# Kernel tuning notes

Measured on AMD Instinct MI355X. Metric: run time of the kernel, lower is better.

The kernel has to match this reference:

```python
import jax, jax.numpy as jnp
import numpy as np

B, T, DI, D = 8, 256, 64, 128
PRED_LEN, OUT_DIM = 96, 7
LN_EPS = 1e-5


def setup_inputs() -> dict:
    key = jax.random.key(0)
    ks = jax.random.split(key, 10)
    s = lambda k, shape, sc: (jax.random.normal(k, shape, jnp.float32) * sc)
    return {
        'x': s(ks[0], (B, T, DI), 1.0),
        'W_b': s(ks[1], (DI, D), DI ** -0.5), 'b_b': jnp.zeros((D,), jnp.float32),
        'Wk': s(ks[2], (D, D), D ** -0.5),
        'Wv': s(ks[3], (D, D), D ** -0.5),
        'Wq': s(ks[4], (D, D), D ** -0.5),
        'W_m': s(ks[5], (D, 3), D ** -0.5), 'b_m': jnp.zeros((3,), jnp.float32),
        'W_f': s(ks[6], (2 * D, D), (2 * D) ** -0.5), 'b_f': jnp.zeros((D,), jnp.float32),
        'W1': s(ks[7], (D, D), D ** -0.5), 'b1': jnp.zeros((D,), jnp.float32),
        'g1': jnp.ones((D,), jnp.float32), 'be1': jnp.zeros((D,), jnp.float32),
        'W2': s(ks[8], (D, PRED_LEN * OUT_DIM), D ** -0.5),
        'b2': jnp.zeros((PRED_LEN * OUT_DIM,), jnp.float32),
    }


def _layernorm(h, g, b):
    mu = h.mean(-1, keepdims=True)
    var = jnp.mean((h - mu) ** 2, -1, keepdims=True)
    return (h - mu) * jax.lax.rsqrt(var + LN_EPS) * g + b


def _forward(x, W_b, b_b, Wk, Wv, Wq, W_m, b_m, W_f, b_f, W1, b1, g1, be1, W2, b2):
    # Backbone P: feature extraction -> f_t  [B,T,D]
    f = jax.nn.gelu(x @ W_b + b_b)
    # Meta-learner: per-step (theta_t, eta_t, alpha_t)
    meta = jax.nn.sigmoid(f @ W_m + b_m)               # [B,T,3]
    theta = 0.01 * meta[..., 0]                         # learning rate
    eta = meta[..., 1]                                  # momentum
    alpha = 0.1 * meta[..., 2]                          # forget/decay
    # Key/value/query projections (precomputed; recurrence is in M,S only)
    k = f @ Wk; v = f @ Wv; q = f @ Wq                  # [B,T,D] each
    seq = (jnp.swapaxes(k, 0, 1), jnp.swapaxes(v, 0, 1), jnp.swapaxes(q, 0, 1),
           theta.T, eta.T, alpha.T)                     # time-major
    M0 = jnp.zeros((B, D, D), f.dtype)
    S0 = jnp.zeros((B, D, D), f.dtype)

    def step(carry, inp):
        M, S = carry
        kt, vt, qt, th, et, al = inp
        # grad of 0.5*||M k - v||^2 wrt M  (rank-1 outer product)
        err = jnp.einsum('bij,bj->bi', M, kt) - vt
        grad = jnp.einsum('bi,bj->bij', err, kt)
        S = et[:, None, None] * S - th[:, None, None] * grad
        M = (1.0 - al)[:, None, None] * M + S
        m_t = jnp.einsum('bij,bj->bi', M, qt)           # retrieve
        return (M, S), m_t

    (_, _), m_seq = jax.lax.scan(step, (M0, S0), seq)
    m = jnp.swapaxes(m_seq, 0, 1)                       # [B,T,D]
    # Gated fusion
    gate = jax.nn.sigmoid(jnp.concatenate([f, m], -1) @ W_f + b_f)
    fused = f * gate + m * (1.0 - gate)
    # Prediction head on last timestep (dropout=0 / eval)
    last = fused[:, -1, :]
    h = jax.nn.gelu(_layernorm(last @ W1 + b1, g1, be1))
    out = h @ W2 + b2
    return out.reshape(B, PRED_LEN, OUT_DIM)


def reference(x, W_b, b_b, Wk, Wv, Wq, W_m, b_m, W_f, b_f, W1, b1, g1, be1, W2, b2):
    return _forward(x, W_b, b_b, Wk, Wv, Wq, W_m, b_m, W_f, b_f, W1, b1, g1, be1, W2, b2)
```

## Files before the change

kernel.cpp:

```cpp
#include <hip/hip_runtime.h>
#include <hip/hip_bf16.h>

#define BB 8
#define TT 256
#define DIN 64
#define DD 128

__device__ __forceinline__ float gelu_tanh(float x) {
  float x3 = x * x * x;
  return 0.5f * x * (1.0f + tanhf(0.7978845608028654f * (x + 0.044715f * x3)));
}
__device__ __forceinline__ float sigmoidf(float x) {
  return 1.0f / (1.0f + __expf(-x));
}

template <typename T> __device__ __forceinline__ float getv(const void* p, int i);
template <> __device__ __forceinline__ float getv<float>(const void* p, int i) {
  return ((const float*)p)[i];
}
template <> __device__ __forceinline__ float getv<__hip_bfloat16>(const void* p, int i) {
  return __bfloat162float(((const __hip_bfloat16*)p)[i]);
}

template <typename T>
__device__ __forceinline__ void fmaV(float* acc, uint4 wv, float fc);
template <>
__device__ __forceinline__ void fmaV<float>(float* acc, uint4 wv, float fc) {
  acc[0] += fc * __uint_as_float(wv.x);
  acc[1] += fc * __uint_as_float(wv.y);
  acc[2] += fc * __uint_as_float(wv.z);
  acc[3] += fc * __uint_as_float(wv.w);
}
template <>
__device__ __forceinline__ void fmaV<__hip_bfloat16>(float* acc, uint4 wv,
                                                     float fc) {
  const unsigned int u0 = wv.x, u1 = wv.y, u2 = wv.z, u3 = wv.w;
  acc[0] += fc * __uint_as_float(u0 << 16);
  acc[1] += fc * __uint_as_float(u0 & 0xffff0000u);
  acc[2] += fc * __uint_as_float(u1 << 16);
  acc[3] += fc * __uint_as_float(u1 & 0xffff0000u);
  acc[4] += fc * __uint_as_float(u2 << 16);
  acc[5] += fc * __uint_as_float(u2 & 0xffff0000u);
  acc[6] += fc * __uint_as_float(u3 << 16);
  acc[7] += fc * __uint_as_float(u3 & 0xffff0000u);
}

template <int CTRL>
__device__ __forceinline__ float dpp_add(float x) {
  int s = __builtin_amdgcn_update_dpp(0, __float_as_int(x), CTRL, 0xF, 0xF, true);
  return x + __int_as_float(s);
}

__device__ __forceinline__ float rowsum16(float p) {
  p = dpp_add<0xB1>(p);
  p = dpp_add<0x4E>(p);
  p = dpp_add<0x124>(p);
  p = dpp_add<0x128>(p);
  return p;
}

__device__ __forceinline__ void gload_lds16(const void* g, void* l) {
  __builtin_amdgcn_global_load_lds(
      (const __attribute__((address_space(1))) void*)g,
      (__attribute__((address_space(3))) void*)l, 16, 0, 0);
}

__device__ __forceinline__ int dtype_good(const unsigned short* u, int idx) {
  unsigned int bits = ((unsigned int)u[idx]) << 16;
  float f = __uint_as_float(bits);
  float a = fabsf(f);
  return (a == 0.0f || (a > 1e-4f && a < 100.0f)) ? 1 : 0;
}

template <typename T>
__device__ void k1_body(const void* x, const void* W_b, const void* b_b,
                        const void* Wk, const void* Wv, const void* Wq,
                        const void* W_m, const void* b_m,
                        float* kout, float* vout, float* scal4,
                        float* q_last, float* f_last) {
  constexpr int VEC = (sizeof(T) == 2) ? 8 : 4;
  constexpr int OC = DD / VEC;
  constexpr int SPL = 128 / OC;
  const int row = blockIdx.x;
  const int b = row >> 8, t = row & 255;
  const int tid = threadIdx.x;
  const int oc = tid % OC, s = tid / OC;

  __shared__ float xs[DIN];
  __shared__ float fs[DD];
  __shared__ float partA[128 * DD / 16];
  __shared__ float partB[128 * DD / 16];

  if (tid < DIN) xs[tid] = getv<T>(x, row * DIN + tid);
  __syncthreads();

  float acc[VEC];

#define GEMV_PART(Wp, SRC, R, PART)                                          \
  {                                                                          \
    _Pragma("unroll") for (int j = 0; j < VEC; ++j) acc[j] = 0.0f;           \
    constexpr int rps = (R) / SPL;                                           \
    _Pragma("unroll 4") for (int cc = 0; cc < rps; ++cc) {                   \
      const int c = s * rps + cc;                                            \
      const uint4 wv =                                                       \
          *(const uint4*)((const T*)(Wp) + (size_t)c * DD + oc * VEC);       \
      fmaV<T>(acc, wv, (SRC)[c]);                                            \
    }                                                                        \
    _Pragma("unroll") for (int j = 0; j < VEC; ++j)                          \
        (PART)[s * DD + oc * VEC + j] = acc[j];                              \
  }

  GEMV_PART(W_b, xs, DIN, partA);
  __syncthreads();
  if (tid < DD) {
    float a = getv<T>(b_b, tid);
#pragma unroll
    for (int ss = 0; ss < SPL; ++ss) a += partA[ss * DD + tid];
    fs[tid] = gelu_tanh(a);
  }
  __syncthreads();

  GEMV_PART(Wk, fs, DD, partA);
  GEMV_PART(Wv, fs, DD, partB);
  __syncthreads();
  if (tid < DD) {
    float ak = 0.0f, av = 0.0f;
#pragma unroll
    for (int ss = 0; ss < SPL; ++ss) {
      ak += partA[ss * DD + tid];
      av += partB[ss * DD + tid];
    }
    kout[row * DD + tid] = ak;
    vout[row * DD + tid] = av;
  }

  if (tid < 64) {
    float a3[3];
#pragma unroll
    for (int j = 0; j < 3; ++j) {
      float pj = fs[tid] * getv<T>(W_m, tid * 3 + j) +
                 fs[tid + 64] * getv<T>(W_m, (tid + 64) * 3 + j);
      pj = rowsum16(pj);
      pj += __shfl_xor(pj, 16);
      pj += __shfl_xor(pj, 32);
      a3[j] = pj;
    }
    if (tid == 0) {
      scal4[row * 4 + 0] = 0.01f * sigmoidf(a3[0] + getv<T>(b_m, 0));
      scal4[row * 4 + 1] = sigmoidf(a3[1] + getv<T>(b_m, 1));
      scal4[row * 4 + 2] = 0.1f * sigmoidf(a3[2] + getv<T>(b_m, 2));
      scal4[row * 4 + 3] = 0.0f;
    }
  }

  if (t == TT - 1) {
    __syncthreads();
    GEMV_PART(Wq, fs, DD, partA);
    __syncthreads();
    if (tid < DD) {
      float aq = 0.0f;
#pragma unroll
      for (int ss = 0; ss < SPL; ++ss) aq += partA[ss * DD + tid];
      q_last[b * DD + tid] = aq;
      f_last[b * DD + tid] = fs[tid];
    }
  }
#undef GEMV_PART
}

__global__ __launch_bounds__(128) void k1_kern(
    const void* x, const void* W_b, const void* b_b, const void* Wk,
    const void* Wv, const void* Wq, const void* W_m, const void* b_m,
    float* kout, float* vout, float* scal4, float* q_last, float* f_last) {
  __shared__ int gcnt[2];
  {
    const int tid = threadIdx.x;
    const unsigned short* u = (const unsigned short*)x;
    int good = 0;
#pragma unroll
    for (int j = 0; j < 16; ++j) good += dtype_good(u, j * 128 + tid);
    float gf = (float)good;
    gf = rowsum16(gf);
    gf += __shfl_xor(gf, 16);
    gf += __shfl_xor(gf, 32);
    if ((tid & 63) == 0) gcnt[tid >> 6] = (int)(gf + 0.5f);
  }
  __syncthreads();
  const bool isbf16 = (gcnt[0] + gcnt[1] >= 1536);
  __syncthreads();

  if (isbf16)
    k1_body<__hip_bfloat16>(x, W_b, b_b, Wk, Wv, Wq, W_m, b_m, kout, vout,
                            scal4, q_last, f_last);
  else
    k1_body<float>(x, W_b, b_b, Wk, Wv, Wq, W_m, b_m, kout, vout, scal4,
                   q_last, f_last);
}

__global__ __launch_bounds__(64) void k2_scan(
    const float* __restrict__ kbuf, const float* __restrict__ vbuf,
    const float* __restrict__ scal, const float* __restrict__ q_last,
    float* __restrict__ m_last) {
  const int tid = threadIdx.x;
  const int g = tid & 15;
  const int cidx = tid >> 4;
  const int chain = blockIdx.x * 4 + cidx;
  const int b = chain >> 7;
  const int i = chain & 127;
  const int i0 = (blockIdx.x * 4) & 127;

  __shared__ float kl[2][32 * DD];
  __shared__ float vl[TT * 4];
  __shared__ float4 scl[TT];

  const float* kslice = kbuf + (size_t)b * TT * DD;
  const float* vslice = vbuf + (size_t)b * TT * DD;

  for (int idx = tid; idx < TT * 4; idx += 64)
    vl[idx] = vslice[(idx >> 2) * DD + i0 + (idx & 3)];
  const float4* sp4 = (const float4*)scal + b * TT;
  for (int idx = tid; idx < TT; idx += 64) scl[idx] = sp4[idx];

#define K2_GLL(CH, BUF)                                                      \
  {                                                                          \
    const float* gs = kslice + (CH) * 32 * DD + tid * 4;                     \
    _Pragma("unroll") for (int j = 0; j < 16; ++j)                           \
        gload_lds16(gs + j * 256, &kl[BUF][j * 256]);                        \
  }
  K2_GLL(0, 0);

  float4 Ma = {0, 0, 0, 0}, Mb = {0, 0, 0, 0};
  float4 Sa = {0, 0, 0, 0}, Sb = {0, 0, 0, 0};

#define K2_STEP(KA, KB, VV, SC)                                              \
  {                                                                          \
    float p = (Ma.x * KA.x + Ma.y * KA.y) + (Ma.z * KA.z + Ma.w * KA.w) +    \
              (Mb.x * KB.x + Mb.y * KB.y) + (Mb.z * KB.z + Mb.w * KB.w);     \
    p = rowsum16(p);                                                         \
    const float err = p - VV;                                                \
    const float c = SC.x * err;                             \
    const float et = SC.y;                                          \
    const float am = 1.0f - SC.z;                             \
    Sa.x = et * Sa.x - c * KA.x;  Ma.x = am * Ma.x + Sa.x;                   \
    Sa.y = et * Sa.y - c * KA.y;  Ma.y = am * Ma.y + Sa.y;                   \
    Sa.z = et * Sa.z - c * KA.z;  Ma.z = am * Ma.z + Sa.z;                   \
    Sa.w = et * Sa.w - c * KA.w;  Ma.w = am * Ma.w + Sa.w;                   \
    Sb.x = et * Sb.x - c * KB.x;  Mb.x = am * Mb.x + Sb.x;                   \
    Sb.y = et * Sb.y - c * KB.y;  Mb.y = am * Mb.y + Sb.y;                   \
    Sb.z = et * Sb.z - c * KB.z;  Mb.z = am * Mb.z + Sb.z;                   \
    Sb.w = et * Sb.w - c * KB.w;  Mb.w = am * Mb.w + Sb.w;                   \
  }

  for (int ch = 0; ch < 8; ++ch) {
    asm volatile("s_waitcnt vmcnt(0) lgkmcnt(0)" ::: "memory");
    if (ch < 7) K2_GLL(ch + 1, (ch + 1) & 1);

    const float* kc = &kl[ch & 1][0];
    const int tbase = ch * 32;

    float4 ka = *(const float4*)(kc + g * 4);
    float4 kb = *(const float4*)(kc + 64 + g * 4);
    float vv = vl[tbase * 4 + cidx];
    float4 sc = scl[tbase];

#pragma unroll
    for (int tt = 0; tt < 32; ++tt) {
      float4 nka, nkb, nsc;
      float nv;
      if (tt < 31) {
        nka = *(const float4*)(kc + (tt + 1) * DD + g * 4);
        nkb = *(const float4*)(kc + (tt + 1) * DD + 64 + g * 4);
        nv = vl[(tbase + tt + 1) * 4 + cidx];
        nsc = scl[tbase + tt + 1];
      }
      K2_STEP(ka, kb, vv, sc);
      if (tt < 31) { ka = nka; kb = nkb; vv = nv; sc = nsc; }
    }
  }
#undef K2_STEP
#undef K2_GLL

  const float* qb0 = q_last + b * DD;
  float4 qa = *(const float4*)(qb0 + g * 4);
  float4 qb = *(const float4*)(qb0 + 64 + g * 4);
  float p = (Ma.x * qa.x + Ma.y * qa.y) + (Ma.z * qa.z + Ma.w * qa.w) +
            (Mb.x * qb.x + Mb.y * qb.y) + (Mb.z * qb.z + Mb.w * qb.w);
  p = rowsum16(p);
  if (g == 0) m_last[b * DD + i] = p;
}

template <typename T>
__device__ void k3_body(const float* f_last, const float* m_last,
                        const void* W_f, const void* b_f, const void* W1,
                        const void* b1, const void* g1, const void* be1,
                        const void* W2, const void* b2, void* out) {
  constexpr int VEC = (sizeof(T) == 2) ? 8 : 4;
  constexpr int OC = DD / VEC;
  constexpr int SPL = 256 / OC;
  const int b = blockIdx.x / 11;
  const int jc = blockIdx.x % 11;
  const int tid = threadIdx.x;
  const int oc = tid % OC, s = tid / OC;

  __shared__ float fm[2 * DD];
  __shared__ float part[2048];
  __shared__ float fused[DD];
  __shared__ float tmp[DD];
  __shared__ float h[DD];
  __shared__ float smu, srs;

  if (tid < 2 * DD)
    fm[tid] = (tid < DD) ? f_last[b * DD + tid] : m_last[b * DD + tid - DD];
  __syncthreads();

  float acc[VEC];

  {
#pragma unroll
    for (int j = 0; j < VEC; ++j) acc[j] = 0.0f;
    constexpr int rps = 256 / SPL;
#pragma unroll 4
    for (int cc = 0; cc < rps; ++cc) {
      const int c = s * rps + cc;
      const uint4 wv =
          *(const uint4*)((const T*)W_f + (size_t)c * DD + oc * VEC);
      fmaV<T>(acc, wv, fm[c]);
    }
#pragma unroll
    for (int j = 0; j < VEC; ++j) part[s * DD + oc * VEC + j] = acc[j];
  }
  __syncthreads();
  if (tid < DD) {
    float a = getv<T>(b_f, tid);
#pragma unroll
    for (int ss = 0; ss < SPL; ++ss) a += part[ss * DD + tid];
    float gte = sigmoidf(a);
    fused[tid] = fm[tid] * gte + fm[DD + tid] * (1.0f - gte);
  }
  __syncthreads();

  {
#pragma unroll
    for (int j = 0; j < VEC; ++j) acc[j] = 0.0f;
    constexpr int rps = DD / SPL;
#pragma unroll 4
    for (int cc = 0; cc < rps; ++cc) {
      const int c = s * rps + cc;
      const uint4 wv =
          *(const uint4*)((const T*)W1 + (size_t)c * DD + oc * VEC);
      fmaV<T>(acc, wv, fused[c]);
    }
#pragma unroll
    for (int j = 0; j < VEC; ++j) part[s * DD + oc * VEC + j] = acc[j];
  }
  __syncthreads();
  if (tid < DD) {
    float a = getv<T>(b1, tid);
#pragma unroll
    for (int ss = 0; ss < SPL; ++ss) a += part[ss * DD + tid];
    tmp[tid] = a;
  }
  __syncthreads();

  if (tid < 64) {
    float x0 = tmp[tid], x1 = tmp[tid + 64];
    float sm = x0 + x1;
    float sq = x0 * x0 + x1 * x1;
    sm = rowsum16(sm);
    sq = rowsum16(sq);
    sm += __shfl_xor(sm, 16); sq += __shfl_xor(sq, 16);
    sm += __shfl_xor(sm, 32); sq += __shfl_xor(sq, 32);
    if (tid == 0) {
      float mu = sm / (float)DD;
      smu = mu;
      srs = rsqrtf(sq / (float)DD - mu * mu + 1e-5f);
    }
  }
  __syncthreads();

  if (tid < DD)
    h[tid] = gelu_tanh((tmp[tid] - smu) * srs * getv<T>(g1, tid) +
                       getv<T>(be1, tid));
  __syncthreads();

  {
    constexpr int NJ = 64 / VEC;
    constexpr int SPL2 = 256 / NJ;
    constexpr int rps2 = DD / SPL2;
    const int jv = tid % NJ, s2 = tid / NJ;
    const int jbase = jc * 64 + jv * VEC;
#pragma unroll
    for (int j = 0; j < VEC; ++j) acc[j] = 0.0f;
    if (jbase < 672) {
#pragma unroll
      for (int cc = 0; cc < rps2; ++cc) {
        const int c = s2 * rps2 + cc;
        const uint4 wv = *(const uint4*)((const T*)W2 + (size_t)c * 672 + jbase);
        fmaV<T>(acc, wv, h[c]);
      }
    }
#pragma unroll
    for (int j = 0; j < VEC; ++j) part[s2 * 64 + jv * VEC + j] = acc[j];
    __syncthreads();

    const int j = jc * 64 + tid;
    if (tid < 64 && j < 672) {
      float r = getv<T>(b2, j);
#pragma unroll
      for (int ss = 0; ss < SPL2; ++ss) r += part[ss * 64 + tid];
      if (sizeof(T) == 2)
        ((__hip_bfloat16*)out)[b * 672 + j] = __float2bfloat16(r);
      else
        ((float*)out)[b * 672 + j] = r;
    }
  }
}

__global__ __launch_bounds__(256) void k3_kern(
    const void* x, const float* f_last, const float* m_last, const void* W_f,
    const void* b_f, const void* W1, const void* b1, const void* g1,
    const void* be1, const void* W2, const void* b2, void* out) {
  __shared__ int gcnt[4];
  {
    const int tid = threadIdx.x;
    const unsigned short* u = (const unsigned short*)x;
    int good = 0;
#pragma unroll
    for (int j = 0; j < 8; ++j) good += dtype_good(u, j * 256 + tid);
    float gf = (float)good;
    gf = rowsum16(gf);
    gf += __shfl_xor(gf, 16);
    gf += __shfl_xor(gf, 32);
    if ((tid & 63) == 0) gcnt[tid >> 6] = (int)(gf + 0.5f);
  }
  __syncthreads();
  const bool isbf16 = (gcnt[0] + gcnt[1] + gcnt[2] + gcnt[3] >= 1536);
  __syncthreads();

  if (isbf16)
    k3_body<__hip_bfloat16>(f_last, m_last, W_f, b_f, W1, b1, g1, be1, W2, b2,
                            out);
  else
    k3_body<float>(f_last, m_last, W_f, b_f, W1, b1, g1, be1, W2, b2, out);
}

extern "C" void kernel_launch(void* const* d_in, const int* in_sizes, int n_in,
                              void* d_out, int out_size, void* d_ws,
                              size_t ws_size, hipStream_t stream) {
  const void* x   = d_in[0];
  const void* W_b = d_in[1];
  const void* b_b = d_in[2];
  const void* Wk  = d_in[3];
  const void* Wv  = d_in[4];
  const void* Wq  = d_in[5];
  const void* W_m = d_in[6];
  const void* b_m = d_in[7];
  const void* W_f = d_in[8];
  const void* b_f = d_in[9];
  const void* W1  = d_in[10];
  const void* b1  = d_in[11];
  const void* g1  = d_in[12];
  const void* be1 = d_in[13];
  const void* W2  = d_in[14];
  const void* b2  = d_in[15];

  float* w = (float*)d_ws;
  float* kbuf   = w;
  float* vbuf   = w + 262144;
  float* scal4  = w + 524288;
  float* q_last = w + 532480;
  float* f_last = w + 533504;
  float* m_last = w + 534528;

  k1_kern<<<BB * TT, 128, 0, stream>>>(x, W_b, b_b, Wk, Wv, Wq, W_m, b_m,
                                       kbuf, vbuf, scal4, q_last, f_last);
  k2_scan<<<256, 64, 0, stream>>>(kbuf, vbuf, scal4, q_last, m_last);
  k3_kern<<<88, 256, 0, stream>>>(x, f_last, m_last, W_f, b_f, W1, b1, g1,
                                  be1, W2, b2, d_out);
}
```

Measured before the change: 144.9 us.

## Break recurrence dependency by computing M·k from lagged M, S dot products

Rewrites the sequential delta-rule recurrence so the prediction M_t·k_t is built algebraically from the previous step's M and S dotted with k, plus a k_prev·k term. The three dot products and their cross-lane reductions can then run in parallel with the rank-1 update of the previous step, instead of the reduction sitting directly on the M update critical path. In exchange there are three reductions per step instead of one, extra registers, and a slightly different floating-point summation order.

```diff
diff --git a/kernel.cpp b/kernel.cpp
--- a/kernel.cpp
+++ b/kernel.cpp
@@ -231,24 +231,31 @@
 
   float4 Ma = {0, 0, 0, 0}, Mb = {0, 0, 0, 0};
   float4 Sa = {0, 0, 0, 0}, Sb = {0, 0, 0, 0};
-
-#define K2_STEP(KA, KB, VV, SC)                                              \
+  float4 kpa = {0, 0, 0, 0}, kpb = {0, 0, 0, 0};
+  float DMc = 0.0f, DSc = 0.0f, KKc = 0.0f;
+  float4 sc1 = {0, 0, 0, 0}, sc2 = {0, 0, 0, 0};
+  float v1 = 0.0f;
+  float cP = 0.0f;
+
+  v1 = vl[cidx];
+  sc1 = scl[0];
+
+#define K2_PHASE23()                                                         \
   {                                                                          \
-    float p = (Ma.x * KA.x + Ma.y * KA.y) + (Ma.z * KA.z + Ma.w * KA.w) +    \
-              (Mb.x * KB.x + Mb.y * KB.y) + (Mb.z * KB.z + Mb.w * KB.w);     \
-    p = rowsum16(p);                                                         \
-    const float err = p - VV;                                                \
-    const float c = SC.x * err;                             \
-    const float et = SC.y;                                          \
-    const float am = 1.0f - SC.z;                             \
-    Sa.x = et * Sa.x - c * KA.x;  Ma.x = am * Ma.x + Sa.x;                   \
-    Sa.y = et * Sa.y - c * KA.y;  Ma.y = am * Ma.y + Sa.y;                   \
-    Sa.z = et * Sa.z - c * KA.z;  Ma.z = am * Ma.z + Sa.z;                   \
-    Sa.w = et * Sa.w - c * KA.w;  Ma.w = am * Ma.w + Sa.w;                   \
-    Sb.x = et * Sb.x - c * KB.x;  Mb.x = am * Mb.x + Sb.x;                   \
-    Sb.y = et * Sb.y - c * KB.y;  Mb.y = am * Mb.y + Sb.y;                   \
-    Sb.z = et * Sb.z - c * KB.z;  Mb.z = am * Mb.z + Sb.z;                   \
-    Sb.w = et * Sb.w - c * KB.w;  Mb.w = am * Mb.w + Sb.w;                   \
+    const float am2 = 1.0f - sc2.z, et2 = sc2.y;                             \
+    const float p = am2 * DMc + et2 * DSc - cP * KKc;                        \
+    const float err = p - v1;                                                \
+    const float c = sc1.x * err;                                             \
+    const float et1 = sc1.y, am1 = 1.0f - sc1.z;                             \
+    Sa.x = et1 * Sa.x - c * kpa.x;  Ma.x = am1 * Ma.x + Sa.x;                \
+    Sa.y = et1 * Sa.y - c * kpa.y;  Ma.y = am1 * Ma.y + Sa.y;                \
+    Sa.z = et1 * Sa.z - c * kpa.z;  Ma.z = am1 * Ma.z + Sa.z;                \
+    Sa.w = et1 * Sa.w - c * kpa.w;  Ma.w = am1 * Ma.w + Sa.w;                \
+    Sb.x = et1 * Sb.x - c * kpb.x;  Mb.x = am1 * Mb.x + Sb.x;                \
+    Sb.y = et1 * Sb.y - c * kpb.y;  Mb.y = am1 * Mb.y + Sb.y;                \
+    Sb.z = et1 * Sb.z - c * kpb.z;  Mb.z = am1 * Mb.z + Sb.z;                \
+    Sb.w = et1 * Sb.w - c * kpb.w;  Mb.w = am1 * Mb.w + Sb.w;                \
+    cP = c;                                                                  \
   }
 
   for (int ch = 0; ch < 8; ++ch) {
@@ -258,26 +265,36 @@
     const float* kc = &kl[ch & 1][0];
     const int tbase = ch * 32;
 
-    float4 ka = *(const float4*)(kc + g * 4);
-    float4 kb = *(const float4*)(kc + 64 + g * 4);
-    float vv = vl[tbase * 4 + cidx];
-    float4 sc = scl[tbase];
-
 #pragma unroll
     for (int tt = 0; tt < 32; ++tt) {
-      float4 nka, nkb, nsc;
-      float nv;
-      if (tt < 31) {
-        nka = *(const float4*)(kc + (tt + 1) * DD + g * 4);
-        nkb = *(const float4*)(kc + (tt + 1) * DD + 64 + g * 4);
-        nv = vl[(tbase + tt + 1) * 4 + cidx];
-        nsc = scl[tbase + tt + 1];
+      const int j = tbase + tt;
+      float4 ka = *(const float4*)(kc + tt * DD + g * 4);
+      float4 kb = *(const float4*)(kc + tt * DD + 64 + g * 4);
+      float dm = (Ma.x * ka.x + Ma.y * ka.y) + (Ma.z * ka.z + Ma.w * ka.w) +
+                 (Mb.x * kb.x + Mb.y * kb.y) + (Mb.z * kb.z + Mb.w * kb.w);
+      float ds = (Sa.x * ka.x + Sa.y * ka.y) + (Sa.z * ka.z + Sa.w * ka.w) +
+                 (Sb.x * kb.x + Sb.y * kb.y) + (Sb.z * kb.z + Sb.w * kb.w);
+      float kk = (kpa.x * ka.x + kpa.y * ka.y) + (kpa.z * ka.z + kpa.w * ka.w) +
+                 (kpb.x * kb.x + kpb.y * kb.y) + (kpb.z * kb.z + kpb.w * kb.w);
+      dm = rowsum16(dm);
+      ds = rowsum16(ds);
+      kk = rowsum16(kk);
+      float vCur = vl[j * 4 + cidx];
+      float4 scCur = scl[j];
+
+      if (tt > 0) {
+        K2_PHASE23();
+      } else if (ch > 0) {
+        K2_PHASE23();
       }
-      K2_STEP(ka, kb, vv, sc);
-      if (tt < 31) { ka = nka; kb = nkb; vv = nv; sc = nsc; }
-    }
-  }
-#undef K2_STEP
+
+      DMc = dm; DSc = ds; KKc = kk;
+      sc2 = sc1; sc1 = scCur; v1 = vCur;
+      kpa = ka; kpb = kb;
+    }
+  }
+  K2_PHASE23();
+#undef K2_PHASE23
 #undef K2_GLL
 
   const float* qb0 = q_last + b * DD;
```

Result: slower. 158.5 us (+9.4%).
